# Kernel optimization log

Measured on AMD Instinct MI355X. Metric: run time of the kernel, lower is better.

## Reference

```python
import jax, jax.numpy as jnp
import numpy as np

T = 16384      # trajectory length
Z = 8          # num_zones
DIN = 8        # person_attrs_dim
E = 16         # num edges
PENALTY = 1000.0
DIFFUSION_STRENGTH = 0.2
EPS = 1e-20


def setup_inputs() -> dict:
    key = jax.random.key(0)
    ks = jax.random.split(key, 20)
    s = 0.05  # weight scale
    return {
        "person_attrs": jax.random.normal(ks[0], (DIN,), jnp.float32),
        "times": jnp.arange(T, dtype=jnp.float32),
        "gumbel_u": jax.random.uniform(ks[1], (T, Z), jnp.float32),
        "edge_index": jax.random.randint(ks[2], (2, E), 0, Z),
        "W1": jax.random.normal(ks[3], (256, DIN + 1 + Z), jnp.float32) * s,
        "b1": jnp.zeros((256,), jnp.float32),
        "W2": jax.random.normal(ks[4], (128, 256), jnp.float32) * s,
        "b2": jnp.zeros((128,), jnp.float32),
        "W3": jax.random.normal(ks[5], (64, 128), jnp.float32) * s,
        "b3": jnp.zeros((64,), jnp.float32),
        "W4": jax.random.normal(ks[6], (Z, 64), jnp.float32) * s,
        "b4": jnp.zeros((Z,), jnp.float32),
        "D1": jax.random.normal(ks[7], (128, DIN + 1), jnp.float32) * s,
        "d1": jnp.zeros((128,), jnp.float32),
        "D2": jax.random.normal(ks[8], (64, 128), jnp.float32) * s,
        "d2": jnp.zeros((64,), jnp.float32),
        "D3": jax.random.normal(ks[9], (Z, 64), jnp.float32) * s,
        "d3": jnp.zeros((Z,), jnp.float32),
        "tau": jnp.asarray(1.0, jnp.float32),
    }


def _adjacency(edge_index, num_zones):
    A = jnp.zeros((num_zones, num_zones), jnp.float32)
    A = A.at[edge_index[0], edge_index[1]].set(1.0)
    A = A.at[edge_index[1], edge_index[0]].set(1.0)
    d = jnp.arange(num_zones)
    return A.at[d, d].set(1.0)


def _forward(person_attrs, times, gumbel_u, W1, b1, W2, b2, W3, b3, W4, b4,
             D1, d1, D2, d2, D3, d3, tau, edge_index):
    num_zones = W4.shape[0]
    din = person_attrs.shape[0]
    A = _adjacency(edge_index, num_zones)

    # normalized time: times / times[-1] if times[-1] > 0 else 0
    last = times[-1]
    denom = jnp.where(last > 0, last, jnp.asarray(1.0, times.dtype))
    norm_t = jnp.where(last > 0, times / denom, jnp.zeros_like(times))  # [T]

    # Precompute (attrs, time)-dependent parts batched over all timesteps.
    # trajectory_net layer 1 split: columns [0:din]=attrs, [din]=time, [din+1:]=zone one-hot
    f_base = person_attrs @ W1[:, :din].T + norm_t[:, None] * W1[:, din][None, :] + b1  # [T,256]
    W1z = W1[:, din + 1:]  # [256, Z]

    # diversity_net depends only on (attrs, time): batch it fully.
    h = jax.nn.relu(person_attrs @ D1[:, :din].T + norm_t[:, None] * D1[:, din][None, :] + d1)  # [T,128]
    h = jax.nn.relu(h @ D2.T + d2)                                                              # [T,64]
    diversity = jnp.tanh(h @ D3.T + d3)                                                         # [T,Z]

    gumbels = -jnp.log(-jnp.log(gumbel_u + EPS) + EPS)  # [T,Z]

    zone0 = jax.nn.one_hot(0, num_zones, dtype=jnp.float32)

    def step(zone_soft, xs):
        f1, dv, g = xs
        h1 = jax.nn.relu(f1 + W1z @ zone_soft)
        h2 = jax.nn.relu(W2 @ h1 + b2)
        h3 = jax.nn.relu(W3 @ h2 + b3)
        base_logits = W4 @ h3 + b4
        combined = base_logits + DIFFUSION_STRENGTH * dv
        cur = jnp.argmax(zone_soft)
        constrained = combined - PENALTY * (1.0 - A[cur])
        y = jax.nn.softmax((constrained + g) / tau)
        nxt = jnp.argmax(y)
        hard = jax.nn.one_hot(nxt, num_zones, dtype=y.dtype)
        zone_next = y + jax.lax.stop_gradient(hard - y)  # straight-through hard gumbel
        return zone_next, (constrained, nxt)

    _, (traj_logits, traj_zones) = jax.lax.scan(step, zone0, (f_base, diversity, gumbels))
    return traj_logits, traj_zones


def reference(person_attrs, times, gumbel_u, edge_index, W1, b1, W2, b2, W3, b3,
              W4, b4, D1, d1, D2, d2, D3, d3, tau):
    return _forward(person_attrs, times, gumbel_u, W1, b1, W2, b2, W3, b3, W4, b4,
                    D1, d1, D2, d2, D3, d3, tau, edge_index)
```

## Files before the change

### kernel.cpp

```cpp
#include <hip/hip_runtime.h>
#include <cstdint>

#define T_STEPS 16384

#define WS_U     0
#define WS_V     256
#define WS_W1ZT  512
#define WS_PEN   2560
#define WS_A     2624
#define WS_W4T   2688
#define WS_W2T   3968
#define WS_W3T   36736
#define WS_DV    53120
#define WS_G     184192
#define WS_CONS  315264
#define WS_ABT   1363840
#define WS_A4LR  1888128
#define WS_H3LR  1920896
#define WS_END_F 2183040
#define WSB_NXT8 ((size_t)WS_END_F * 4)
#define WSB_CUR  (WSB_NXT8 + 131072)
#define WSB_CRX  (WSB_CUR + 65536)

#define PB_W2T   128
#define PB_W3T   (PB_W2T + 32)
#define PB_GUM   (PB_W3T + 512)
#define PB_SETUP PB_GUM
#define NB_PREP  (PB_SETUP + 1)

__device__ __forceinline__ unsigned int fn_compose(unsigned int hi, unsigned int lo) {
  unsigned int r = 0;
  #pragma unroll
  for (int x = 0; x < 8; ++x) {
    unsigned int m = (lo >> (3 * x)) & 7u;
    r |= ((hi >> (3 * m)) & 7u) << (3 * x);
  }
  return r;
}

__global__ void __launch_bounds__(256) k_prep(
    const float* __restrict__ pa, const float* __restrict__ gum,
    const int* __restrict__ edge,
    const float* __restrict__ W1, const float* __restrict__ b1,
    const float* __restrict__ W2, const float* __restrict__ W3,
    const float* __restrict__ W4,
    float* __restrict__ ws) {
  int b = blockIdx.x, tid = threadIdx.x;
  if (b < PB_W2T) {
    int e = b * 256 + tid;
    int k = e >> 7, j = e & 127;
    ws[WS_W2T + e] = W2[j * 256 + k];
  } else if (b < PB_W3T) {
    int e = (b - PB_W2T) * 256 + tid;
    int i = e & 63, j = e >> 6;
    ws[WS_W3T + e] = W3[i * 128 + j];
  } else if (b < PB_GUM) {
    int e = (b - PB_W3T) * 256 + tid;
    float uu = gum[e];
    ws[WS_G + e] = -logf(-logf(uu + 1e-20f) + 1e-20f);
  } else {
    {
      int k = tid;
      float acc = b1[k];
      #pragma unroll
      for (int i = 0; i < 8; ++i) acc = fmaf(pa[i], W1[k * 17 + i], acc);
      ws[WS_U + k] = acc;
      ws[WS_V + k] = W1[k * 17 + 8];
    }
    for (int e = tid; e < 2048; e += 256) {
      int cc = e >> 8, k = e & 255;
      ws[WS_W1ZT + e] = W1[k * 17 + 9 + cc];
    }
    for (int e = tid; e < 512; e += 256) {
      int k = e >> 3, z = e & 7;
      ws[WS_W4T + e] = W4[z * 64 + k];
    }
    if (tid < 64) ws[WS_A + tid] = ((tid >> 3) == (tid & 7)) ? 1.0f : 0.0f;
    __syncthreads();
    if (tid == 0) {
      for (int e = 0; e < 16; ++e) {
        int aa = edge[e], bb = edge[16 + e];
        ws[WS_A + aa * 8 + bb] = 1.0f;
        ws[WS_A + bb * 8 + aa] = 1.0f;
      }
    }
    __syncthreads();
    if (tid < 64) ws[WS_PEN + tid] = 1000.0f * (1.0f - ws[WS_A + tid]);
  }
}

__global__ void __launch_bounds__(256) k_div(
    const float* __restrict__ pa, const float* __restrict__ times,
    const float* __restrict__ D1, const float* __restrict__ d1,
    const float* __restrict__ D2, const float* __restrict__ d2,
    const float* __restrict__ D3, const float* __restrict__ d3,
    float* __restrict__ ws) {
  __shared__ float sD2[64 * 128];
  __shared__ float sudc[128], svdc[128];
  __shared__ float part[3][8][64];
  int tid = threadIdx.x;
  int lane = tid & 63;
  int w = __builtin_amdgcn_readfirstlane(tid >> 6);
  int t = blockIdx.x * 64 + lane;
  float last = times[T_STEPS - 1];
  float st = (last > 0.0f) ? times[t] / last : 0.0f;

  #pragma unroll
  for (int i = 0; i < 8; ++i)
    ((float4*)sD2)[i * 256 + tid] = ((const float4*)D2)[i * 256 + tid];
  if (tid < 128) {
    float acc = d1[tid];
    #pragma unroll
    for (int i = 0; i < 8; ++i) acc = fmaf(pa[i], D1[tid * 9 + i], acc);
    sudc[tid] = acc;
    svdc[tid] = D1[tid * 9 + 8];
  }
  __syncthreads();

  int j0 = __builtin_amdgcn_readfirstlane(w * 16);
  float accj[16];
  #pragma unroll
  for (int jj = 0; jj < 16; ++jj) accj[jj] = d2[j0 + jj];
  #pragma unroll 4
  for (int k = 0; k < 128; ++k) {
    float h1 = fmaxf(fmaf(st, svdc[k], sudc[k]), 0.0f);
    #pragma unroll
    for (int jj = 0; jj < 16; ++jj)
      accj[jj] = fmaf(sD2[(j0 + jj) * 128 + k], h1, accj[jj]);
  }
  float dvp[8];
  #pragma unroll
  for (int z = 0; z < 8; ++z) dvp[z] = (w == 0) ? d3[z] : 0.0f;
  #pragma unroll
  for (int jj = 0; jj < 16; ++jj) {
    float h2 = fmaxf(accj[jj], 0.0f);
    #pragma unroll
    for (int z = 0; z < 8; ++z)
      dvp[z] = fmaf(D3[z * 64 + j0 + jj], h2, dvp[z]);
  }
  if (w > 0) {
    #pragma unroll
    for (int z = 0; z < 8; ++z) part[w - 1][z][lane] = dvp[z];
  }
  __syncthreads();
  if (w == 0) {
    #pragma unroll
    for (int z = 0; z < 8; ++z) {
      float dvv = dvp[z] + part[0][z][lane] + part[1][z][lane] + part[2][z][lane];
      ws[WS_DV + t * 8 + z] = tanhf(dvv);
    }
  }
}

__global__ void __launch_bounds__(256) k_ab4(
    const float* __restrict__ times,
    const float* __restrict__ u_, const float* __restrict__ v_,
    const float* __restrict__ w1zt, const float* __restrict__ w2t,
    const float* __restrict__ w3t, const float* __restrict__ w4t,
    const float* __restrict__ b2, const float* __restrict__ b3,
    const float* __restrict__ b4,
    float* __restrict__ abt, int* __restrict__ crx,
    float* __restrict__ a4lr, float* __restrict__ h3lr) {
  __shared__ float s_au[256], s_av[256];
  __shared__ float s_pa[128], s_pb[128];
  __shared__ unsigned long long s_bal[4];
  __shared__ float s_h2L[128], s_h2R[128];
  __shared__ float s_h3pL[4][64], s_h3pR[4][64];
  __shared__ float s_h3L[64], s_h3R[64];
  __shared__ int s_d2, s_d3, s_cnt;
  int blk = blockIdx.x;
  int c = blk >> 8, tile = blk & 255;
  int tid = threadIdx.x;
  float last = times[T_STEPS - 1];
  float stL = (last > 0.0f) ? times[tile * 64] / last : 0.0f;
  float stR = (last > 0.0f) ? times[tile * 64 + 63] / last : 0.0f;
  {
    float uk = u_[tid] + w1zt[c * 256 + tid];
    float vk = v_[tid];
    float valL = fmaf(stL, vk, uk);
    float valR = fmaf(stR, vk, uk);
    float mn = fminf(valL, valR);
    float mx = fmaxf(valL, valR);
    bool act = (mn > 0.0f);
    bool cross = (!act) && (mx > 0.0f);
    s_au[tid] = act ? uk : 0.0f;
    s_av[tid] = act ? vk : 0.0f;
    unsigned long long bal = __ballot(cross);
    if ((tid & 63) == 0) s_bal[tid >> 6] = bal;
  }
  if (tid == 0) { s_d2 = 0; s_d3 = 0; }
  __syncthreads();
  if (tid == 0) {
    int cnt = 0;
    int list8[8];
    #pragma unroll
    for (int i = 0; i < 8; ++i) list8[i] = 0;
    #pragma unroll
    for (int w = 0; w < 4; ++w) {
      unsigned long long m = s_bal[w];
      while (m) {
        int bit = __ffsll(m) - 1;
        if (cnt < 8) list8[cnt] = w * 64 + bit;
        ++cnt;
        m &= (m - 1);
      }
    }
    crx[blk * 12] = cnt;
    s_cnt = cnt;
    #pragma unroll
    for (int i = 0; i < 8; ++i) crx[blk * 12 + 1 + i] = list8[i];
  }
  {
    int j = tid & 127, half = tid >> 7;
    float A = 0.0f, B = 0.0f;
    const float* wrow = w2t + half * 128 * 128 + j;
    int kb = half * 128;
    #pragma unroll 4
    for (int kk = 0; kk < 128; ++kk) {
      float w = wrow[kk * 128];
      A = fmaf(s_au[kb + kk], w, A);
      B = fmaf(s_av[kb + kk], w, B);
    }
    if (half == 1) { s_pa[j] = A; s_pb[j] = B; }
    __syncthreads();
    if (half == 0) {
      float Af = A + s_pa[j] + b2[j];
      float Bf = B + s_pb[j];
      abt[(size_t)blk * 256 + j * 2]     = Af;
      abt[(size_t)blk * 256 + j * 2 + 1] = Bf;
      float preL = fmaf(stL, Bf, Af);
      float preR = fmaf(stR, Bf, Af);
      if ((preL > 0.0f) != (preR > 0.0f)) atomicOr(&s_d2, 1);
      s_h2L[j] = fmaxf(preL, 0.0f);
      s_h2R[j] = fmaxf(preR, 0.0f);
    }
  }
  __syncthreads();
  {
    int i = tid & 63, jq = tid >> 6;
    float aL = (jq == 0) ? b3[i] : 0.0f;
    float aR = aL;
    int j0 = jq * 32;
    #pragma unroll 4
    for (int jj = 0; jj < 32; ++jj) {
      float w = w3t[(j0 + jj) * 64 + i];
      aL = fmaf(w, s_h2L[j0 + jj], aL);
      aR = fmaf(w, s_h2R[j0 + jj], aR);
    }
    s_h3pL[jq][i] = aL;
    s_h3pR[jq][i] = aR;
  }
  __syncthreads();
  if (tid < 64) {
    float preL = s_h3pL[0][tid] + s_h3pL[1][tid] + s_h3pL[2][tid] + s_h3pL[3][tid];
    float preR = s_h3pR[0][tid] + s_h3pR[1][tid] + s_h3pR[2][tid] + s_h3pR[3][tid];
    if ((preL > 0.0f) != (preR > 0.0f)) atomicOr(&s_d3, 1);
    s_h3L[tid] = fmaxf(preL, 0.0f);
    s_h3R[tid] = fmaxf(preR, 0.0f);
    h3lr[(size_t)blk * 128 + tid]      = preL;
    h3lr[(size_t)blk * 128 + 64 + tid] = preR;
  }
  __syncthreads();
  if (tid < 8) {
    float aL = b4[tid], aR = b4[tid];
    #pragma unroll 8
    for (int i = 0; i < 64; ++i) {
      float w = w4t[i * 8 + tid];
      aL = fmaf(w, s_h3L[i], aL);
      aR = fmaf(w, s_h3R[i], aR);
    }
    a4lr[blk * 16 + tid]     = aL;
    a4lr[blk * 16 + 8 + tid] = aR;
  }
  if (tid == 0) {
    int flag = 0;
    if (s_cnt == 0 && s_d2 == 0) flag = s_d3 ? 2 : 1;
    crx[blk * 12 + 9] = flag;
  }
}

__global__ void __launch_bounds__(256, 8) k_mlp(
    const float* __restrict__ times,
    const float* __restrict__ u_, const float* __restrict__ v_,
    const float* __restrict__ w1zt, const float* __restrict__ w2t,
    const float* __restrict__ abt, const int* __restrict__ crx,
    const float* __restrict__ a4lr, const float* __restrict__ h3lr,
    const float* __restrict__ w3t, const float* __restrict__ w4t,
    const float* __restrict__ b2, const float* __restrict__ b3,
    const float* __restrict__ b4,
    const float* __restrict__ dv, const float* __restrict__ gt,
    const float* __restrict__ pen, const float* __restrict__ tau,
    float* __restrict__ cons_out, unsigned char* __restrict__ nxt_out) {
  __shared__ float part[3][8][64];
  int tid = threadIdx.x;
  int lane = tid & 63;
  int iq = __builtin_amdgcn_readfirstlane(tid >> 6);
  int blk = blockIdx.x;
  int c = blk >> 8, tgrp = blk & 255;
  int t = tgrp * 64 + lane;
  int abase = blk * 256;
  int cbase = blk * 12;
  int flag = crx[cbase + 9];

  if (flag == 1) {
    if (iq == 0) {
      float frac = (float)lane * (1.0f / 63.0f);
      float a4[8];
      #pragma unroll
      for (int z = 0; z < 8; ++z) {
        float L = a4lr[blk * 16 + z];
        float R = a4lr[blk * 16 + 8 + z];
        a4[z] = fmaf(frac, R - L, L);
      }
      float4 dv0 = *(const float4*)(dv + (size_t)t * 8);
      float4 dv1 = *(const float4*)(dv + (size_t)t * 8 + 4);
      float4 g0  = *(const float4*)(gt + (size_t)t * 8);
      float4 g1  = *(const float4*)(gt + (size_t)t * 8 + 4);
      float dvv[8] = {dv0.x, dv0.y, dv0.z, dv0.w, dv1.x, dv1.y, dv1.z, dv1.w};
      float gv[8]  = {g0.x, g0.y, g0.z, g0.w, g1.x, g1.y, g1.z, g1.w};
      float sgn = (tau[0] > 0.0f) ? 1.0f : -1.0f;
      float cons[8];
      float best = 0.0f; int bz = 0;
      #pragma unroll
      for (int z = 0; z < 8; ++z) {
        float lg = fmaf(0.2f, dvv[z], a4[z]) - pen[c * 8 + z];
        cons[z] = lg;
        float yv = (lg + gv[z]) * sgn;
        if (z == 0) { best = yv; bz = 0; }
        else if (yv > best) { best = yv; bz = z; }
      }
      float* co = cons_out + ((size_t)t * 8 + c) * 8;
      *(float4*)co = make_float4(cons[0], cons[1], cons[2], cons[3]);
      *(float4*)(co + 4) = make_float4(cons[4], cons[5], cons[6], cons[7]);
      nxt_out[t * 8 + c] = (unsigned char)bz;
    }
    return;
  }

  float last = times[T_STEPS - 1];
  float st = (last > 0.0f) ? times[t] / last : 0.0f;
  const float* w1c = w1zt + c * 256;
  int cnt = crx[cbase];

  float acc[16];
  if (flag == 2) {
    float frac = (float)lane * (1.0f / 63.0f);
    #pragma unroll
    for (int i = 0; i < 16; ++i) {
      float L = h3lr[(size_t)blk * 128 + iq * 16 + i];
      float R = h3lr[(size_t)blk * 128 + 64 + iq * 16 + i];
      acc[i] = fmaf(frac, R - L, L);
    }
  } else {
    #pragma unroll
    for (int i = 0; i < 16; ++i) acc[i] = b3[iq * 16 + i];
    const float* w3 = w3t + iq * 16;

    if (cnt == 0) {
      #pragma unroll 4
      for (int j = 0; j < 128; ++j) {
        float A = abt[abase + j * 2];
        float B = abt[abase + j * 2 + 1];
        float h2 = fmaxf(fmaf(st, B, A), 0.0f);
        #pragma unroll
        for (int i = 0; i < 16; ++i)
          acc[i] = fmaf(w3[j * 64 + i], h2, acc[i]);
      }
    } else if (cnt <= 8) {
      int kk[8];
      #pragma unroll
      for (int i = 0; i < 8; ++i) kk[i] = (i < cnt) ? crx[cbase + 1 + i] : 0;
      float hx[8];
      #pragma unroll
      for (int i = 0; i < 8; ++i)
        hx[i] = (i < cnt) ? fmaxf(fmaf(st, v_[kk[i]], u_[kk[i]] + w1c[kk[i]]), 0.0f) : 0.0f;
      #pragma unroll 2
      for (int j = 0; j < 128; ++j) {
        float A = abt[abase + j * 2];
        float B = abt[abase + j * 2 + 1];
        float h2p = fmaf(st, B, A);
        #pragma unroll
        for (int i = 0; i < 8; ++i)
          h2p = fmaf(hx[i], w2t[kk[i] * 128 + j], h2p);
        float h2 = fmaxf(h2p, 0.0f);
        #pragma unroll
        for (int i = 0; i < 16; ++i)
          acc[i] = fmaf(w3[j * 64 + i], h2, acc[i]);
      }
    } else {
      for (int j = 0; j < 128; ++j) {
        float h2p = b2[j];
        for (int k = 0; k < 256; ++k) {
          float h1 = fmaxf(fmaf(st, v_[k], u_[k] + w1c[k]), 0.0f);
          h2p = fmaf(w2t[k * 128 + j], h1, h2p);
        }
        float h2 = fmaxf(h2p, 0.0f);
        #pragma unroll
        for (int i = 0; i < 16; ++i)
          acc[i] = fmaf(w3[j * 64 + i], h2, acc[i]);
      }
    }
  }

  float p[8];
  #pragma unroll
  for (int z = 0; z < 8; ++z) p[z] = (iq == 0) ? b4[z] : 0.0f;
  #pragma unroll 4
  for (int i = 0; i < 16; ++i) {
    float h3 = fmaxf(acc[i], 0.0f);
    #pragma unroll
    for (int z = 0; z < 8; ++z)
      p[z] = fmaf(w4t[(iq * 16 + i) * 8 + z], h3, p[z]);
  }
  if (iq > 0) {
    #pragma unroll
    for (int z = 0; z < 8; ++z) part[iq - 1][z][lane] = p[z];
  }
  __syncthreads();
  if (iq == 0) {
    float a4[8];
    #pragma unroll
    for (int z = 0; z < 8; ++z)
      a4[z] = p[z] + part[0][z][lane] + part[1][z][lane] + part[2][z][lane];
    float4 dv0 = *(const float4*)(dv + (size_t)t * 8);
    float4 dv1 = *(const float4*)(dv + (size_t)t * 8 + 4);
    float4 g0  = *(const float4*)(gt + (size_t)t * 8);
    float4 g1  = *(const float4*)(gt + (size_t)t * 8 + 4);
    float dvv[8] = {dv0.x, dv0.y, dv0.z, dv0.w, dv1.x, dv1.y, dv1.z, dv1.w};
    float gv[8]  = {g0.x, g0.y, g0.z, g0.w, g1.x, g1.y, g1.z, g1.w};
    float sgn = (tau[0] > 0.0f) ? 1.0f : -1.0f;
    float cons[8];
    float best = 0.0f; int bz = 0;
    #pragma unroll
    for (int z = 0; z < 8; ++z) {
      float lg = fmaf(0.2f, dvv[z], a4[z]) - pen[c * 8 + z];
      cons[z] = lg;
      float yv = (lg + gv[z]) * sgn;
      if (z == 0) { best = yv; bz = 0; }
      else if (yv > best) { best = yv; bz = z; }
    }
    float* co = cons_out + ((size_t)t * 8 + c) * 8;
    *(float4*)co = make_float4(cons[0], cons[1], cons[2], cons[3]);
    *(float4*)(co + 4) = make_float4(cons[4], cons[5], cons[6], cons[7]);
    nxt_out[t * 8 + c] = (unsigned char)bz;
  }
}

__global__ void __launch_bounds__(1024) k_phaseC(float* __restrict__ ws, float* __restrict__ d_out) {
  int tid = threadIdx.x;
  const unsigned char* nxt8 = (const unsigned char*)ws + WSB_NXT8;
  unsigned int* cur_arr = (unsigned int*)((char*)ws + WSB_CUR);
  const unsigned int IDENT = 0x00FAC688u;
  unsigned int f[16];
  int t0 = tid * 16;
  unsigned int F = IDENT;
  #pragma unroll
  for (int i = 0; i < 16; ++i) {
    uint2 b = *(const uint2*)(nxt8 + (size_t)(t0 + i) * 8);
    unsigned int fn = 0;
    #pragma unroll
    for (int q = 0; q < 4; ++q) fn |= ((b.x >> (8 * q)) & 7u) << (3 * q);
    #pragma unroll
    for (int q = 0; q < 4; ++q) fn |= ((b.y >> (8 * q)) & 7u) << (3 * (q + 4));
    f[i] = fn;
    F = fn_compose(fn, F);
  }
  __shared__ unsigned int sc[1024];
  sc[tid] = F;
  __syncthreads();
  #pragma unroll
  for (int d = 1; d < 1024; d <<= 1) {
    unsigned int v = sc[tid];
    unsigned int p = (tid >= d) ? sc[tid - d] : 0u;
    unsigned int nv = (tid >= d) ? fn_compose(v, p) : v;
    __syncthreads();
    sc[tid] = nv;
    __syncthreads();
  }
  unsigned int E = (tid == 0) ? IDENT : sc[tid - 1];
  unsigned int state = E & 7u;
  #pragma unroll
  for (int i = 0; i < 16; ++i) {
    int tt = t0 + i;
    cur_arr[tt] = state;
    unsigned int nx = (f[i] >> (3 * state)) & 7u;
    d_out[131072 + tt] = (float)nx;
    state = nx;
  }
}

__global__ void k_gather(const float* __restrict__ ws, float* __restrict__ d_out) {
  int idx = blockIdx.x * 256 + threadIdx.x;
  const unsigned int* cur_arr = (const unsigned int*)((const char*)ws + WSB_CUR);
  int t = idx >> 3, z = idx & 7;
  unsigned int cur = cur_arr[t];
  d_out[idx] = ws[WS_CONS + (t * 8 + (int)cur) * 8 + z];
}

extern "C" void kernel_launch(void* const* d_in, const int* in_sizes, int n_in,
                              void* d_out, int out_size, void* d_ws, size_t ws_size,
                              hipStream_t stream) {
  const float* pa    = (const float*)d_in[0];
  const float* times = (const float*)d_in[1];
  const float* gum   = (const float*)d_in[2];
  const int*   edge  = (const int*)d_in[3];
  const float* W1  = (const float*)d_in[4];
  const float* b1  = (const float*)d_in[5];
  const float* W2  = (const float*)d_in[6];
  const float* b2  = (const float*)d_in[7];
  const float* W3  = (const float*)d_in[8];
  const float* b3  = (const float*)d_in[9];
  const float* W4  = (const float*)d_in[10];
  const float* b4  = (const float*)d_in[11];
  const float* D1  = (const float*)d_in[12];
  const float* d1v = (const float*)d_in[13];
  const float* D2  = (const float*)d_in[14];
  const float* d2v = (const float*)d_in[15];
  const float* D3  = (const float*)d_in[16];
  const float* d3v = (const float*)d_in[17];
  const float* tau = (const float*)d_in[18];
  float* ws = (float*)d_ws;
  float* out = (float*)d_out;
  int* crx = (int*)((char*)d_ws + WSB_CRX);

  k_prep<<<NB_PREP, 256, 0, stream>>>(pa, gum, edge, W1, b1, W2, W3, W4, ws);
  k_div<<<256, 256, 0, stream>>>(pa, times, D1, d1v, D2, d2v, D3, d3v, ws);
  k_ab4<<<2048, 256, 0, stream>>>(times, ws + WS_U, ws + WS_V, ws + WS_W1ZT,
                                  ws + WS_W2T, ws + WS_W3T, ws + WS_W4T,
                                  b2, b3, b4, ws + WS_ABT, crx,
                                  ws + WS_A4LR, ws + WS_H3LR);
  k_mlp<<<2048, 256, 0, stream>>>(times, ws + WS_U, ws + WS_V, ws + WS_W1ZT,
                                  ws + WS_W2T, ws + WS_ABT, crx,
                                  ws + WS_A4LR, ws + WS_H3LR,
                                  ws + WS_W3T, ws + WS_W4T, b2, b3, b4,
                                  ws + WS_DV, ws + WS_G, ws + WS_PEN, tau,
                                  ws + WS_CONS, (unsigned char*)ws + WSB_NXT8);
  k_phaseC<<<1, 1024, 0, stream>>>(ws, out);
  k_gather<<<512, 256, 0, stream>>>(ws, out);
}
```

Measured before the change: 90.69 us.

## Fuse prep with diversity kernel and ab4 with mlp kernel via shared memory

Merges k_prep and k_div into one launch, and merges k_ab4 and k_mlp so the per-block A/B coefficients, crossing lists, endpoint activations and flags stay in LDS and never round-trip through global workspace. W3 is staged into shared memory and read as float4 vectors in the inner loops. This removes two launches and the intermediate global traffic. The cost is much larger LDS use per block (about 40KB) and a lower launch-bounds occupancy target, which may reduce the number of resident blocks.

```diff
diff --git a/kernel.cpp b/kernel.cpp
--- a/kernel.cpp
+++ b/kernel.cpp
@@ -14,18 +14,15 @@
 #define WS_DV    53120
 #define WS_G     184192
 #define WS_CONS  315264
-#define WS_ABT   1363840
-#define WS_A4LR  1888128
-#define WS_H3LR  1920896
-#define WS_END_F 2183040
+#define WS_END_F 1363840
 #define WSB_NXT8 ((size_t)WS_END_F * 4)
 #define WSB_CUR  (WSB_NXT8 + 131072)
-#define WSB_CRX  (WSB_CUR + 65536)
-
-#define PB_W2T   128
-#define PB_W3T   (PB_W2T + 32)
-#define PB_GUM   (PB_W3T + 512)
-#define PB_SETUP PB_GUM
+
+#define PB_DIV   0
+#define PB_W2T   256
+#define PB_W3T   (PB_W2T + 128)
+#define PB_GUM   (PB_W3T + 32)
+#define PB_SETUP (PB_GUM + 512)
 #define NB_PREP  (PB_SETUP + 1)
 
 __device__ __forceinline__ unsigned int fn_compose(unsigned int hi, unsigned int lo) {
@@ -38,59 +35,12 @@
   return r;
 }
 
-__global__ void __launch_bounds__(256) k_prep(
-    const float* __restrict__ pa, const float* __restrict__ gum,
-    const int* __restrict__ edge,
+__global__ void __launch_bounds__(256) k_prepdiv(
+    const float* __restrict__ pa, const float* __restrict__ times,
+    const float* __restrict__ gum, const int* __restrict__ edge,
     const float* __restrict__ W1, const float* __restrict__ b1,
     const float* __restrict__ W2, const float* __restrict__ W3,
     const float* __restrict__ W4,
-    float* __restrict__ ws) {
-  int b = blockIdx.x, tid = threadIdx.x;
-  if (b < PB_W2T) {
-    int e = b * 256 + tid;
-    int k = e >> 7, j = e & 127;
-    ws[WS_W2T + e] = W2[j * 256 + k];
-  } else if (b < PB_W3T) {
-    int e = (b - PB_W2T) * 256 + tid;
-    int i = e & 63, j = e >> 6;
-    ws[WS_W3T + e] = W3[i * 128 + j];
-  } else if (b < PB_GUM) {
-    int e = (b - PB_W3T) * 256 + tid;
-    float uu = gum[e];
-    ws[WS_G + e] = -logf(-logf(uu + 1e-20f) + 1e-20f);
-  } else {
-    {
-      int k = tid;
-      float acc = b1[k];
-      #pragma unroll
-      for (int i = 0; i < 8; ++i) acc = fmaf(pa[i], W1[k * 17 + i], acc);
-      ws[WS_U + k] = acc;
-      ws[WS_V + k] = W1[k * 17 + 8];
-    }
-    for (int e = tid; e < 2048; e += 256) {
-      int cc = e >> 8, k = e & 255;
-      ws[WS_W1ZT + e] = W1[k * 17 + 9 + cc];
-    }
-    for (int e = tid; e < 512; e += 256) {
-      int k = e >> 3, z = e & 7;
-      ws[WS_W4T + e] = W4[z * 64 + k];
-    }
-    if (tid < 64) ws[WS_A + tid] = ((tid >> 3) == (tid & 7)) ? 1.0f : 0.0f;
-    __syncthreads();
-    if (tid == 0) {
-      for (int e = 0; e < 16; ++e) {
-        int aa = edge[e], bb = edge[16 + e];
-        ws[WS_A + aa * 8 + bb] = 1.0f;
-        ws[WS_A + bb * 8 + aa] = 1.0f;
-      }
-    }
-    __syncthreads();
-    if (tid < 64) ws[WS_PEN + tid] = 1000.0f * (1.0f - ws[WS_A + tid]);
-  }
-}
-
-__global__ void __launch_bounds__(256) k_div(
-    const float* __restrict__ pa, const float* __restrict__ times,
     const float* __restrict__ D1, const float* __restrict__ d1,
     const float* __restrict__ D2, const float* __restrict__ d2,
     const float* __restrict__ D3, const float* __restrict__ d3,
@@ -98,82 +48,133 @@
   __shared__ float sD2[64 * 128];
   __shared__ float sudc[128], svdc[128];
   __shared__ float part[3][8][64];
-  int tid = threadIdx.x;
-  int lane = tid & 63;
-  int w = __builtin_amdgcn_readfirstlane(tid >> 6);
-  int t = blockIdx.x * 64 + lane;
-  float last = times[T_STEPS - 1];
-  float st = (last > 0.0f) ? times[t] / last : 0.0f;
-
-  #pragma unroll
-  for (int i = 0; i < 8; ++i)
-    ((float4*)sD2)[i * 256 + tid] = ((const float4*)D2)[i * 256 + tid];
-  if (tid < 128) {
-    float acc = d1[tid];
-    #pragma unroll
-    for (int i = 0; i < 8; ++i) acc = fmaf(pa[i], D1[tid * 9 + i], acc);
-    sudc[tid] = acc;
-    svdc[tid] = D1[tid * 9 + 8];
-  }
-  __syncthreads();
-
-  int j0 = __builtin_amdgcn_readfirstlane(w * 16);
-  float accj[16];
-  #pragma unroll
-  for (int jj = 0; jj < 16; ++jj) accj[jj] = d2[j0 + jj];
-  #pragma unroll 4
-  for (int k = 0; k < 128; ++k) {
-    float h1 = fmaxf(fmaf(st, svdc[k], sudc[k]), 0.0f);
-    #pragma unroll
-    for (int jj = 0; jj < 16; ++jj)
-      accj[jj] = fmaf(sD2[(j0 + jj) * 128 + k], h1, accj[jj]);
-  }
-  float dvp[8];
-  #pragma unroll
-  for (int z = 0; z < 8; ++z) dvp[z] = (w == 0) ? d3[z] : 0.0f;
-  #pragma unroll
-  for (int jj = 0; jj < 16; ++jj) {
-    float h2 = fmaxf(accj[jj], 0.0f);
-    #pragma unroll
-    for (int z = 0; z < 8; ++z)
-      dvp[z] = fmaf(D3[z * 64 + j0 + jj], h2, dvp[z]);
-  }
-  if (w > 0) {
-    #pragma unroll
-    for (int z = 0; z < 8; ++z) part[w - 1][z][lane] = dvp[z];
-  }
-  __syncthreads();
-  if (w == 0) {
-    #pragma unroll
-    for (int z = 0; z < 8; ++z) {
-      float dvv = dvp[z] + part[0][z][lane] + part[1][z][lane] + part[2][z][lane];
-      ws[WS_DV + t * 8 + z] = tanhf(dvv);
-    }
+  int b = blockIdx.x, tid = threadIdx.x;
+  if (b < PB_W2T) {
+    int lane = tid & 63;
+    int w = __builtin_amdgcn_readfirstlane(tid >> 6);
+    int t = b * 64 + lane;
+    float last = times[T_STEPS - 1];
+    float st = (last > 0.0f) ? times[t] / last : 0.0f;
+    #pragma unroll
+    for (int i = 0; i < 8; ++i)
+      ((float4*)sD2)[i * 256 + tid] = ((const float4*)D2)[i * 256 + tid];
+    if (tid < 128) {
+      float acc = d1[tid];
+      #pragma unroll
+      for (int i = 0; i < 8; ++i) acc = fmaf(pa[i], D1[tid * 9 + i], acc);
+      sudc[tid] = acc;
+      svdc[tid] = D1[tid * 9 + 8];
+    }
+    __syncthreads();
+    int j0 = __builtin_amdgcn_readfirstlane(w * 16);
+    float accj[16];
+    #pragma unroll
+    for (int jj = 0; jj < 16; ++jj) accj[jj] = d2[j0 + jj];
+    #pragma unroll 4
+    for (int k = 0; k < 128; ++k) {
+      float h1 = fmaxf(fmaf(st, svdc[k], sudc[k]), 0.0f);
+      #pragma unroll
+      for (int jj = 0; jj < 16; ++jj)
+        accj[jj] = fmaf(sD2[(j0 + jj) * 128 + k], h1, accj[jj]);
+    }
+    float dvp[8];
+    #pragma unroll
+    for (int z = 0; z < 8; ++z) dvp[z] = (w == 0) ? d3[z] : 0.0f;
+    #pragma unroll
+    for (int jj = 0; jj < 16; ++jj) {
+      float h2 = fmaxf(accj[jj], 0.0f);
+      #pragma unroll
+      for (int z = 0; z < 8; ++z)
+        dvp[z] = fmaf(D3[z * 64 + j0 + jj], h2, dvp[z]);
+    }
+    if (w > 0) {
+      #pragma unroll
+      for (int z = 0; z < 8; ++z) part[w - 1][z][lane] = dvp[z];
+    }
+    __syncthreads();
+    if (w == 0) {
+      #pragma unroll
+      for (int z = 0; z < 8; ++z) {
+        float dvv = dvp[z] + part[0][z][lane] + part[1][z][lane] + part[2][z][lane];
+        ws[WS_DV + t * 8 + z] = tanhf(dvv);
+      }
+    }
+  } else if (b < PB_W3T) {
+    int e = (b - PB_W2T) * 256 + tid;
+    int k = e >> 7, j = e & 127;
+    ws[WS_W2T + e] = W2[j * 256 + k];
+  } else if (b < PB_GUM) {
+    int e = (b - PB_W3T) * 256 + tid;
+    int i = e & 63, j = e >> 6;
+    ws[WS_W3T + e] = W3[i * 128 + j];
+  } else if (b < PB_SETUP) {
+    int e = (b - PB_GUM) * 256 + tid;
+    float uu = gum[e];
+    ws[WS_G + e] = -logf(-logf(uu + 1e-20f) + 1e-20f);
+  } else {
+    {
+      int k = tid;
+      float acc = b1[k];
+      #pragma unroll
+      for (int i = 0; i < 8; ++i) acc = fmaf(pa[i], W1[k * 17 + i], acc);
+      ws[WS_U + k] = acc;
+      ws[WS_V + k] = W1[k * 17 + 8];
+    }
+    for (int e = tid; e < 2048; e += 256) {
+      int cc = e >> 8, k = e & 255;
+      ws[WS_W1ZT + e] = W1[k * 17 + 9 + cc];
+    }
+    for (int e = tid; e < 512; e += 256) {
+      int k = e >> 3, z = e & 7;
+      ws[WS_W4T + e] = W4[z * 64 + k];
+    }
+    if (tid < 64) ws[WS_A + tid] = ((tid >> 3) == (tid & 7)) ? 1.0f : 0.0f;
+    __syncthreads();
+    if (tid == 0) {
+      for (int e = 0; e < 16; ++e) {
+        int aa = edge[e], bb = edge[16 + e];
+        ws[WS_A + aa * 8 + bb] = 1.0f;
+        ws[WS_A + bb * 8 + aa] = 1.0f;
+      }
+    }
+    __syncthreads();
+    if (tid < 64) ws[WS_PEN + tid] = 1000.0f * (1.0f - ws[WS_A + tid]);
   }
 }
 
-__global__ void __launch_bounds__(256) k_ab4(
+__global__ void __launch_bounds__(256, 3) k_abmlp(
     const float* __restrict__ times,
     const float* __restrict__ u_, const float* __restrict__ v_,
     const float* __restrict__ w1zt, const float* __restrict__ w2t,
     const float* __restrict__ w3t, const float* __restrict__ w4t,
     const float* __restrict__ b2, const float* __restrict__ b3,
     const float* __restrict__ b4,
-    float* __restrict__ abt, int* __restrict__ crx,
-    float* __restrict__ a4lr, float* __restrict__ h3lr) {
+    const float* __restrict__ dv, const float* __restrict__ gt,
+    const float* __restrict__ pen, const float* __restrict__ tau,
+    float* __restrict__ cons_out, unsigned char* __restrict__ nxt_out) {
   __shared__ float s_au[256], s_av[256];
   __shared__ float s_pa[128], s_pb[128];
   __shared__ unsigned long long s_bal[4];
+  __shared__ float s_AB[256];
   __shared__ float s_h2L[128], s_h2R[128];
   __shared__ float s_h3pL[4][64], s_h3pR[4][64];
+  __shared__ float s_preL[64], s_preR[64];
   __shared__ float s_h3L[64], s_h3R[64];
-  __shared__ int s_d2, s_d3, s_cnt;
+  __shared__ float s_a4L[8], s_a4R[8];
+  __shared__ float part[3][8][64];
+  __shared__ float s_w3[8192];
+  __shared__ int s_d2, s_d3, s_cnt, s_flag;
+  __shared__ int s_list[8];
+
   int blk = blockIdx.x;
   int c = blk >> 8, tile = blk & 255;
   int tid = threadIdx.x;
+  int lane = tid & 63;
+  int iq = __builtin_amdgcn_readfirstlane(tid >> 6);
   float last = times[T_STEPS - 1];
   float stL = (last > 0.0f) ? times[tile * 64] / last : 0.0f;
   float stR = (last > 0.0f) ? times[tile * 64 + 63] / last : 0.0f;
+
   {
     float uk = u_[tid] + w1zt[c * 256 + tid];
     float vk = v_[tid];
@@ -205,10 +206,9 @@
         m &= (m - 1);
       }
     }
-    crx[blk * 12] = cnt;
     s_cnt = cnt;
     #pragma unroll
-    for (int i = 0; i < 8; ++i) crx[blk * 12 + 1 + i] = list8[i];
+    for (int i = 0; i < 8; ++i) s_list[i] = list8[i];
   }
   {
     int j = tid & 127, half = tid >> 7;
@@ -226,8 +226,8 @@
     if (half == 0) {
       float Af = A + s_pa[j] + b2[j];
       float Bf = B + s_pb[j];
-      abt[(size_t)blk * 256 + j * 2]     = Af;
-      abt[(size_t)blk * 256 + j * 2 + 1] = Bf;
+      s_AB[j * 2]     = Af;
+      s_AB[j * 2 + 1] = Bf;
       float preL = fmaf(stL, Bf, Af);
       float preR = fmaf(stR, Bf, Af);
       if ((preL > 0.0f) != (preR > 0.0f)) atomicOr(&s_d2, 1);
@@ -255,10 +255,10 @@
     float preL = s_h3pL[0][tid] + s_h3pL[1][tid] + s_h3pL[2][tid] + s_h3pL[3][tid];
     float preR = s_h3pR[0][tid] + s_h3pR[1][tid] + s_h3pR[2][tid] + s_h3pR[3][tid];
     if ((preL > 0.0f) != (preR > 0.0f)) atomicOr(&s_d3, 1);
+    s_preL[tid] = preL;
+    s_preR[tid] = preR;
     s_h3L[tid] = fmaxf(preL, 0.0f);
     s_h3R[tid] = fmaxf(preR, 0.0f);
-    h3lr[(size_t)blk * 128 + tid]      = preL;
-    h3lr[(size_t)blk * 128 + 64 + tid] = preR;
   }
   __syncthreads();
   if (tid < 8) {
@@ -269,49 +269,26 @@
       aL = fmaf(w, s_h3L[i], aL);
       aR = fmaf(w, s_h3R[i], aR);
     }
-    a4lr[blk * 16 + tid]     = aL;
-    a4lr[blk * 16 + 8 + tid] = aR;
+    s_a4L[tid] = aL;
+    s_a4R[tid] = aR;
   }
   if (tid == 0) {
     int flag = 0;
     if (s_cnt == 0 && s_d2 == 0) flag = s_d3 ? 2 : 1;
-    crx[blk * 12 + 9] = flag;
-  }
-}
-
-__global__ void __launch_bounds__(256, 8) k_mlp(
-    const float* __restrict__ times,
-    const float* __restrict__ u_, const float* __restrict__ v_,
-    const float* __restrict__ w1zt, const float* __restrict__ w2t,
-    const float* __restrict__ abt, const int* __restrict__ crx,
-    const float* __restrict__ a4lr, const float* __restrict__ h3lr,
-    const float* __restrict__ w3t, const float* __restrict__ w4t,
-    const float* __restrict__ b2, const float* __restrict__ b3,
-    const float* __restrict__ b4,
-    const float* __restrict__ dv, const float* __restrict__ gt,
-    const float* __restrict__ pen, const float* __restrict__ tau,
-    float* __restrict__ cons_out, unsigned char* __restrict__ nxt_out) {
-  __shared__ float part[3][8][64];
-  int tid = threadIdx.x;
-  int lane = tid & 63;
-  int iq = __builtin_amdgcn_readfirstlane(tid >> 6);
-  int blk = blockIdx.x;
-  int c = blk >> 8, tgrp = blk & 255;
-  int t = tgrp * 64 + lane;
-  int abase = blk * 256;
-  int cbase = blk * 12;
-  int flag = crx[cbase + 9];
+    s_flag = flag;
+  }
+  __syncthreads();
+
+  int flag = s_flag;
+  int t = tile * 64 + lane;
 
   if (flag == 1) {
     if (iq == 0) {
       float frac = (float)lane * (1.0f / 63.0f);
       float a4[8];
       #pragma unroll
-      for (int z = 0; z < 8; ++z) {
-        float L = a4lr[blk * 16 + z];
-        float R = a4lr[blk * 16 + 8 + z];
-        a4[z] = fmaf(frac, R - L, L);
-      }
+      for (int z = 0; z < 8; ++z)
+        a4[z] = fmaf(frac, s_a4R[z] - s_a4L[z], s_a4L[z]);
       float4 dv0 = *(const float4*)(dv + (size_t)t * 8);
       float4 dv1 = *(const float4*)(dv + (size_t)t * 8 + 4);
       float4 g0  = *(const float4*)(gt + (size_t)t * 8);
@@ -337,55 +314,77 @@
     return;
   }
 
-  float last = times[T_STEPS - 1];
   float st = (last > 0.0f) ? times[t] / last : 0.0f;
   const float* w1c = w1zt + c * 256;
-  int cnt = crx[cbase];
+  int cnt = s_cnt;
+  int i0 = iq * 16;
 
   float acc[16];
   if (flag == 2) {
     float frac = (float)lane * (1.0f / 63.0f);
     #pragma unroll
     for (int i = 0; i < 16; ++i) {
-      float L = h3lr[(size_t)blk * 128 + iq * 16 + i];
-      float R = h3lr[(size_t)blk * 128 + 64 + iq * 16 + i];
+      float L = s_preL[i0 + i];
+      float R = s_preR[i0 + i];
       acc[i] = fmaf(frac, R - L, L);
     }
   } else {
-    #pragma unroll
-    for (int i = 0; i < 16; ++i) acc[i] = b3[iq * 16 + i];
-    const float* w3 = w3t + iq * 16;
+    {
+      const float4* w3v = (const float4*)w3t;
+      float4* sw3 = (float4*)s_w3;
+      #pragma unroll
+      for (int r = 0; r < 8; ++r) sw3[r * 256 + tid] = w3v[r * 256 + tid];
+    }
+    __syncthreads();
+    #pragma unroll
+    for (int i = 0; i < 16; ++i) acc[i] = b3[i0 + i];
 
     if (cnt == 0) {
-      #pragma unroll 4
+      #pragma unroll 2
       for (int j = 0; j < 128; ++j) {
-        float A = abt[abase + j * 2];
-        float B = abt[abase + j * 2 + 1];
-        float h2 = fmaxf(fmaf(st, B, A), 0.0f);
-        #pragma unroll
-        for (int i = 0; i < 16; ++i)
-          acc[i] = fmaf(w3[j * 64 + i], h2, acc[i]);
+        float2 ab = *(const float2*)(s_AB + j * 2);
+        float h2 = fmaxf(fmaf(st, ab.y, ab.x), 0.0f);
+        float4 w0 = *(const float4*)(s_w3 + j * 64 + i0);
+        float4 w1 = *(const float4*)(s_w3 + j * 64 + i0 + 4);
+        float4 w2 = *(const float4*)(s_w3 + j * 64 + i0 + 8);
+        float4 w3_ = *(const float4*)(s_w3 + j * 64 + i0 + 12);
+        acc[0] = fmaf(w0.x, h2, acc[0]);  acc[1] = fmaf(w0.y, h2, acc[1]);
+        acc[2] = fmaf(w0.z, h2, acc[2]);  acc[3] = fmaf(w0.w, h2, acc[3]);
+        acc[4] = fmaf(w1.x, h2, acc[4]);  acc[5] = fmaf(w1.y, h2, acc[5]);
+        acc[6] = fmaf(w1.z, h2, acc[6]);  acc[7] = fmaf(w1.w, h2, acc[7]);
+        acc[8] = fmaf(w2.x, h2, acc[8]);  acc[9] = fmaf(w2.y, h2, acc[9]);
+        acc[10] = fmaf(w2.z, h2, acc[10]); acc[11] = fmaf(w2.w, h2, acc[11]);
+        acc[12] = fmaf(w3_.x, h2, acc[12]); acc[13] = fmaf(w3_.y, h2, acc[13]);
+        acc[14] = fmaf(w3_.z, h2, acc[14]); acc[15] = fmaf(w3_.w, h2, acc[15]);
       }
     } else if (cnt <= 8) {
       int kk[8];
       #pragma unroll
-      for (int i = 0; i < 8; ++i) kk[i] = (i < cnt) ? crx[cbase + 1 + i] : 0;
+      for (int i = 0; i < 8; ++i) kk[i] = (i < cnt) ? s_list[i] : 0;
       float hx[8];
       #pragma unroll
       for (int i = 0; i < 8; ++i)
         hx[i] = (i < cnt) ? fmaxf(fmaf(st, v_[kk[i]], u_[kk[i]] + w1c[kk[i]]), 0.0f) : 0.0f;
       #pragma unroll 2
       for (int j = 0; j < 128; ++j) {
-        float A = abt[abase + j * 2];
-        float B = abt[abase + j * 2 + 1];
-        float h2p = fmaf(st, B, A);
+        float2 ab = *(const float2*)(s_AB + j * 2);
+        float h2p = fmaf(st, ab.y, ab.x);
         #pragma unroll
         for (int i = 0; i < 8; ++i)
           h2p = fmaf(hx[i], w2t[kk[i] * 128 + j], h2p);
         float h2 = fmaxf(h2p, 0.0f);
-        #pragma unroll
-        for (int i = 0; i < 16; ++i)
-          acc[i] = fmaf(w3[j * 64 + i], h2, acc[i]);
+        float4 w0 = *(const float4*)(s_w3 + j * 64 + i0);
+        float4 w1 = *(const float4*)(s_w3 + j * 64 + i0 + 4);
+        float4 w2_ = *(const float4*)(s_w3 + j * 64 + i0 + 8);
+        float4 w3_ = *(const float4*)(s_w3 + j * 64 + i0 + 12);
+        acc[0] = fmaf(w0.x, h2, acc[0]);  acc[1] = fmaf(w0.y, h2, acc[1]);
+        acc[2] = fmaf(w0.z, h2, acc[2]);  acc[3] = fmaf(w0.w, h2, acc[3]);
+        acc[4] = fmaf(w1.x, h2, acc[4]);  acc[5] = fmaf(w1.y, h2, acc[5]);
+        acc[6] = fmaf(w1.z, h2, acc[6]);  acc[7] = fmaf(w1.w, h2, acc[7]);
+        acc[8] = fmaf(w2_.x, h2, acc[8]);  acc[9] = fmaf(w2_.y, h2, acc[9]);
+        acc[10] = fmaf(w2_.z, h2, acc[10]); acc[11] = fmaf(w2_.w, h2, acc[11]);
+        acc[12] = fmaf(w3_.x, h2, acc[12]); acc[13] = fmaf(w3_.y, h2, acc[13]);
+        acc[14] = fmaf(w3_.z, h2, acc[14]); acc[15] = fmaf(w3_.w, h2, acc[15]);
       }
     } else {
       for (int j = 0; j < 128; ++j) {
@@ -397,7 +396,7 @@
         float h2 = fmaxf(h2p, 0.0f);
         #pragma unroll
         for (int i = 0; i < 16; ++i)
-          acc[i] = fmaf(w3[j * 64 + i], h2, acc[i]);
+          acc[i] = fmaf(s_w3[j * 64 + i0 + i], h2, acc[i]);
       }
     }
   }
@@ -410,7 +409,7 @@
     float h3 = fmaxf(acc[i], 0.0f);
     #pragma unroll
     for (int z = 0; z < 8; ++z)
-      p[z] = fmaf(w4t[(iq * 16 + i) * 8 + z], h3, p[z]);
+      p[z] = fmaf(w4t[(i0 + i) * 8 + z], h3, p[z]);
   }
   if (iq > 0) {
     #pragma unroll
@@ -521,20 +520,14 @@
   const float* tau = (const float*)d_in[18];
   float* ws = (float*)d_ws;
   float* out = (float*)d_out;
-  int* crx = (int*)((char*)d_ws + WSB_CRX);
-
-  k_prep<<<NB_PREP, 256, 0, stream>>>(pa, gum, edge, W1, b1, W2, W3, W4, ws);
-  k_div<<<256, 256, 0, stream>>>(pa, times, D1, d1v, D2, d2v, D3, d3v, ws);
-  k_ab4<<<2048, 256, 0, stream>>>(times, ws + WS_U, ws + WS_V, ws + WS_W1ZT,
-                                  ws + WS_W2T, ws + WS_W3T, ws + WS_W4T,
-                                  b2, b3, b4, ws + WS_ABT, crx,
-                                  ws + WS_A4LR, ws + WS_H3LR);
-  k_mlp<<<2048, 256, 0, stream>>>(times, ws + WS_U, ws + WS_V, ws + WS_W1ZT,
-                                  ws + WS_W2T, ws + WS_ABT, crx,
-                                  ws + WS_A4LR, ws + WS_H3LR,
-                                  ws + WS_W3T, ws + WS_W4T, b2, b3, b4,
-                                  ws + WS_DV, ws + WS_G, ws + WS_PEN, tau,
-                                  ws + WS_CONS, (unsigned char*)ws + WSB_NXT8);
+
+  k_prepdiv<<<NB_PREP, 256, 0, stream>>>(pa, times, gum, edge, W1, b1, W2, W3, W4,
+                                         D1, d1v, D2, d2v, D3, d3v, ws);
+  k_abmlp<<<2048, 256, 0, stream>>>(times, ws + WS_U, ws + WS_V, ws + WS_W1ZT,
+                                    ws + WS_W2T, ws + WS_W3T, ws + WS_W4T,
+                                    b2, b3, b4, ws + WS_DV, ws + WS_G,
+                                    ws + WS_PEN, tau, ws + WS_CONS,
+                                    (unsigned char*)ws + WSB_NXT8);
   k_phaseC<<<1, 1024, 0, stream>>>(ws, out);
   k_gather<<<512, 256, 0, stream>>>(ws, out);
 }
```

New measurement: 93.21 us. +2.8%, slower.
